# Kernel tuning notes

Measured on AMD Instinct MI355X. Metric: run time of the kernel, lower is better.

Reference implementation:

```python
import jax, jax.numpy as jnp
import numpy as np


def setup_inputs() -> dict:
    key = jax.random.key(0)
    kX, kW, kb, ks = jax.random.split(key, 4)
    B, C, H = 32, 3, 64
    D = C * H * H  # 12288, lin_proj is Linear(D, D)
    N = 196        # superpixels
    X = jax.random.normal(kX, (B, C, H, H), dtype=jnp.float32)
    # scale weight like torch default init (~1/sqrt(D)) to keep activations sane
    W = jax.random.normal(kW, (D, D), dtype=jnp.float32) * (1.0 / np.sqrt(D))
    b = jax.random.normal(kb, (D,), dtype=jnp.float32) * 0.01
    seg_map = jax.random.randint(ks, (B, H, H), 0, N, dtype=jnp.int32)
    return {"X": X, "W": W, "b": b, "seg_map": seg_map, "superpixels": N}


def reference(X, W, b, seg_map, superpixels):
    B, C, H, Wd = X.shape
    D = C * H * Wd
    # lin_proj over the fully flattened image (as in the torch module)
    x = X.reshape(B, D) @ W.T + b                      # [B, D]
    x = x.reshape(B, C, H * Wd)                        # back to per-pixel channels
    pix = x.transpose(0, 2, 1).reshape(B * H * Wd, C)  # [B*HW, C]
    # offset segment ids so every image gets its own id range
    ids = (seg_map.reshape(B, H * Wd) + jnp.arange(B, dtype=seg_map.dtype)[:, None] * superpixels).reshape(-1)
    nseg = B * superpixels
    sums = jax.ops.segment_sum(pix, ids, num_segments=nseg)                     # [B*N, C]
    cnts = jax.ops.segment_sum(jnp.ones((ids.shape[0],), x.dtype), ids, num_segments=nseg)
    means = sums / jnp.maximum(cnts, 1.0)[:, None]     # masked mean per superpixel per channel
    return means.reshape(B, superpixels, C)            # [B, N_superpixels, in_chans]
```

## Files before the change

### kernel.cpp

```cpp
#include <hip/hip_runtime.h>


#include <hip/hip_bf16.h>

typedef __attribute__((ext_vector_type(8))) short short8;
typedef __attribute__((ext_vector_type(4))) float f32x4;

namespace {
constexpr int BATCH = 32;
constexpr int CH    = 3;
constexpr int HWPIX = 4096;
constexpr int DDIM  = 12288;
constexpr int KDIM  = 12288;
constexpr int NSEG  = 196;

constexpr int ROWS = 64;
constexpr int BK   = 128;
}

__device__ __forceinline__ unsigned pkbf16(float lo, float hi) {
    __hip_bfloat162 h = __float22bfloat162_rn(make_float2(lo, hi));
    union { __hip_bfloat162 h2; unsigned u; } c; c.h2 = h; return c.u;
}

__device__ __forceinline__ void gload16(const void* g, void* l) {
    __builtin_amdgcn_global_load_lds(
        (const __attribute__((address_space(1))) void*)g,
        (__attribute__((address_space(3))) void*)l, 16, 0, 0);
}

__global__ __launch_bounds__(256) void convert_x_kernel(
    const float* __restrict__ X, ushort* __restrict__ Xb)
{
    const int i = (blockIdx.x * 256 + threadIdx.x) * 4;
    const float4 v = *reinterpret_cast<const float4*>(X + i);
    union { unsigned u[2]; ushort4 q; } o;
    o.u[0] = pkbf16(v.x, v.y);
    o.u[1] = pkbf16(v.z, v.w);
    *reinterpret_cast<ushort4*>(Xb + i) = o.q;
}

template<int KSPLIT>
__global__ __launch_bounds__(256, 2) void gemm_kernel(
    const float* __restrict__ Wg, const ushort* __restrict__ Xb,
    float* __restrict__ xpart)
{
    constexpr int KRANGE = KDIM / KSPLIT;
    constexpr int NTILE  = KRANGE / BK;

    __shared__ float  wl[2][ROWS * BK];
    __shared__ ushort xl[2][BATCH * BK];

    const int t    = threadIdx.x;
    const int lane = t & 63;
    const int w    = t >> 6;
    const int d0   = blockIdx.x * ROWS;
    const int kb   = blockIdx.y * KRANGE;

    f32x4 acc[2];
#pragma unroll
    for (int nt = 0; nt < 2; ++nt) acc[nt] = (f32x4)(0.f);

#define STAGE(buf, tile)                                                     \
    {                                                                        \
        const int k0 = kb + (tile) * BK;                                     \
        _Pragma("unroll")                                                    \
        for (int i = 0; i < 8; ++i) {                                        \
            const int r  = w * 16 + i * 2 + (lane >> 5);                     \
            const int cs = (lane & 31) ^ (r & 7);                            \
            gload16(Wg + (size_t)(d0 + r) * KDIM + k0 + cs * 4,              \
                    &wl[buf][(w * 16 + i * 2) * BK]);                        \
        }                                                                    \
        _Pragma("unroll")                                                    \
        for (int i = 0; i < 2; ++i) {                                        \
            const int xr = w * 8 + i * 4 + (lane >> 4);                      \
            const int cs = (lane & 15) ^ (xr & 7);                           \
            gload16(Xb + (size_t)xr * KDIM + k0 + cs * 8,                    \
                    &xl[buf][(w * 8 + i * 4) * BK]);                         \
        }                                                                    \
    }

#define COMPUTE(buf)                                                         \
    {                                                                        \
        _Pragma("unroll")                                                    \
        for (int kk = 0; kk < 4; ++kk) {                                     \
            const int R  = w * 16 + (lane & 15);                             \
            const int c0 = kk * 8 + (lane >> 4) * 2;      \
            const float4 f0 = *reinterpret_cast<const float4*>(              \
                &wl[buf][R * BK + (((c0    ) ^ (R & 7)) & 31) * 4]);         \
            const float4 f1 = *reinterpret_cast<const float4*>(              \
                &wl[buf][R * BK + (((c0 + 1) ^ (R & 7)) & 31) * 4]);         \
            union { unsigned u[4]; short8 s8; } A;                           \
            A.u[0] = pkbf16(f0.x, f0.y);                                     \
            A.u[1] = pkbf16(f0.z, f0.w);                                     \
            A.u[2] = pkbf16(f1.x, f1.y);                                     \
            A.u[3] = pkbf16(f1.z, f1.w);                                     \
            _Pragma("unroll")                                                \
            for (int nt = 0; nt < 2; ++nt) {                                 \
                const int b  = nt * 16 + (lane & 15);                        \
                const int xc = (kk * 4 + (lane >> 4)) ^ (b & 7);             \
                const short8 bb = *reinterpret_cast<const short8*>(          \
                    &xl[buf][b * BK + xc * 8]);                              \
                acc[nt] = __builtin_amdgcn_mfma_f32_16x16x32_bf16(           \
                    A.s8, bb, acc[nt], 0, 0, 0);                             \
            }                                                                \
        }                                                                    \
    }

    STAGE(0, 0)
    STAGE(1, 1)
    for (int tile = 0; tile < NTILE; ++tile) {
        const int cur = tile & 1;
        if (tile + 1 < NTILE) {
            asm volatile("s_waitcnt vmcnt(10)" ::: "memory");
        } else {
            asm volatile("s_waitcnt vmcnt(0)" ::: "memory");
        }
        __builtin_amdgcn_s_barrier();
        asm volatile("" ::: "memory");
        COMPUTE(cur)
        asm volatile("s_waitcnt lgkmcnt(0)" ::: "memory");
        __builtin_amdgcn_s_barrier();
        asm volatile("" ::: "memory");
        if (tile + 2 < NTILE) STAGE(cur, tile + 2)
    }
#undef STAGE
#undef COMPUTE

    float* xp = xpart + (size_t)blockIdx.y * BATCH * DDIM;
#pragma unroll
    for (int nt = 0; nt < 2; ++nt) {
        const int b = nt * 16 + (lane & 15);
        const int m = d0 + w * 16 + (lane >> 4) * 4;
#pragma unroll
        for (int r = 0; r < 4; ++r)
            xp[(size_t)b * DDIM + m + r] = acc[nt][r];
    }
}

template<int KSPLIT>
__global__ __launch_bounds__(256) void aggregate_kernel(
    const float* __restrict__ xpart, const float* __restrict__ bias,
    const int* __restrict__ seg, float* __restrict__ out)
{
    __shared__ float sums[NSEG];
    __shared__ int   hist[NSEG];
    const int b = blockIdx.x / CH;
    const int c = blockIdx.x % CH;
    for (int i = threadIdx.x; i < NSEG; i += 256) { sums[i] = 0.f; hist[i] = 0; }
    __syncthreads();
    const size_t base = (size_t)b * DDIM + c * HWPIX;
#pragma unroll
    for (int it = 0; it < HWPIX / 1024; ++it) {
        const int p0 = it * 1024 + threadIdx.x * 4;
        const int4 s4 = *reinterpret_cast<const int4*>(seg + b * HWPIX + p0);
        float4 v = *reinterpret_cast<const float4*>(bias + c * HWPIX + p0);
#pragma unroll
        for (int ks = 0; ks < KSPLIT; ++ks) {
            const float4 xv = *reinterpret_cast<const float4*>(
                xpart + (size_t)ks * BATCH * DDIM + base + p0);
            v.x += xv.x; v.y += xv.y; v.z += xv.z; v.w += xv.w;
        }
        atomicAdd(&hist[s4.x], 1); atomicAdd(&sums[s4.x], v.x);
        atomicAdd(&hist[s4.y], 1); atomicAdd(&sums[s4.y], v.y);
        atomicAdd(&hist[s4.z], 1); atomicAdd(&sums[s4.z], v.z);
        atomicAdd(&hist[s4.w], 1); atomicAdd(&sums[s4.w], v.w);
    }
    __syncthreads();
    for (int s = threadIdx.x; s < NSEG; s += 256)
        out[(b * NSEG + s) * CH + c] = sums[s] / fmaxf((float)hist[s], 1.f);
}

extern "C" void kernel_launch(void* const* d_in, const int* in_sizes, int n_in,
                              void* d_out, int out_size, void* d_ws, size_t ws_size,
                              hipStream_t stream) {
    const float* X    = (const float*)d_in[0];
    const float* W    = (const float*)d_in[1];
    const float* bias = (const float*)d_in[2];
    const int*   seg  = (const int*)d_in[3];
    float* out = (float*)d_out;

    ushort* Xb    = (ushort*)d_ws;
    float*  xpart = (float*)(Xb + (size_t)BATCH * KDIM);

    convert_x_kernel<<<BATCH * KDIM / (256 * 4), 256, 0, stream>>>(X, Xb);

    const size_t base_ws = (size_t)BATCH * KDIM * 2;
    const size_t part_ws = (size_t)BATCH * DDIM * 4;
    if (ws_size >= base_ws + 8 * part_ws) {
        dim3 grid(DDIM / ROWS, 8);
        gemm_kernel<8><<<grid, 256, 0, stream>>>(W, Xb, xpart);
        aggregate_kernel<8><<<BATCH * CH, 256, 0, stream>>>(xpart, bias, seg, out);
    } else {
        dim3 grid(DDIM / ROWS, 4);
        gemm_kernel<4><<<grid, 256, 0, stream>>>(W, Xb, xpart);
        aggregate_kernel<4><<<BATCH * CH, 256, 0, stream>>>(xpart, bias, seg, out);
    }
}
```

Measured before the change: 132.7 us.

## Replace grid-level split-K with in-block per-wave K split and LDS reduction

The GEMM drops the global split-K grid dimension and its partial-sum buffers. Each block now owns 16 output rows, and its four waves each walk an interleaved quarter of K with private double-buffered LDS tiles and no block barriers in the main loop. The waves then reduce their results through shared memory and write a single output, so the aggregate kernel reads one array instead of summing 4-8 partials. This removes partial-sum global traffic and per-tile barriers, but the X tile is re-read per block (768 blocks instead of 192x8) and each wave does less MFMA work per load.

```diff
diff --git a/kernel.cpp b/kernel.cpp
--- a/kernel.cpp
+++ b/kernel.cpp
@@ -14,8 +14,10 @@
 constexpr int KDIM  = 12288;
 constexpr int NSEG  = 196;
 
-constexpr int ROWS = 64;
-constexpr int BK   = 128;
+constexpr int ROWS = 16;
+constexpr int BK   = 64;
+constexpr int NCH  = KDIM / BK;
+constexpr int PERW = NCH / 4;
 }
 
 __device__ __forceinline__ unsigned pkbf16(float lo, float hi) {
@@ -40,56 +42,51 @@
     *reinterpret_cast<ushort4*>(Xb + i) = o.q;
 }
 
-template<int KSPLIT>
 __global__ __launch_bounds__(256, 2) void gemm_kernel(
     const float* __restrict__ Wg, const ushort* __restrict__ Xb,
-    float* __restrict__ xpart)
+    float* __restrict__ x)
 {
-    constexpr int KRANGE = KDIM / KSPLIT;
-    constexpr int NTILE  = KRANGE / BK;
+    __shared__ float  wl[4][2][ROWS * BK];
+    __shared__ ushort xl[4][2][BATCH * BK];
+    __shared__ float  red[4][ROWS][BATCH];
 
-    __shared__ float  wl[2][ROWS * BK];
-    __shared__ ushort xl[2][BATCH * BK];
-
-    const int t    = threadIdx.x;
-    const int lane = t & 63;
-    const int w    = t >> 6;
+    const int lane = threadIdx.x & 63;
+    const int w    = threadIdx.x >> 6;
     const int d0   = blockIdx.x * ROWS;
-    const int kb   = blockIdx.y * KRANGE;
 
     f32x4 acc[2];
 #pragma unroll
     for (int nt = 0; nt < 2; ++nt) acc[nt] = (f32x4)(0.f);
 
-#define STAGE(buf, tile)                                                     \
+#define STAGE(buf, c)                                                        \
     {                                                                        \
-        const int k0 = kb + (tile) * BK;                                     \
+        const int k0 = (c) * BK;                                             \
         _Pragma("unroll")                                                    \
-        for (int i = 0; i < 8; ++i) {                                        \
-            const int r  = w * 16 + i * 2 + (lane >> 5);                     \
-            const int cs = (lane & 31) ^ (r & 7);                            \
+        for (int i = 0; i < 4; ++i) {                                        \
+            const int r  = i * 4 + (lane >> 4);                              \
+            const int cs = (lane & 15) ^ (r & 7);                            \
             gload16(Wg + (size_t)(d0 + r) * KDIM + k0 + cs * 4,              \
-                    &wl[buf][(w * 16 + i * 2) * BK]);                        \
+                    &wl[w][buf][i * 4 * BK]);                                \
         }                                                                    \
         _Pragma("unroll")                                                    \
-        for (int i = 0; i < 2; ++i) {                                        \
-            const int xr = w * 8 + i * 4 + (lane >> 4);                      \
-            const int cs = (lane & 15) ^ (xr & 7);                           \
+        for (int i = 0; i < 4; ++i) {                                        \
+            const int xr = i * 8 + (lane >> 3);                              \
+            const int cs = (lane & 7) ^ (xr & 7);                            \
             gload16(Xb + (size_t)xr * KDIM + k0 + cs * 8,                    \
-                    &xl[buf][(w * 8 + i * 4) * BK]);                         \
+                    &xl[w][buf][i * 8 * BK]);                                \
         }                                                                    \
     }
 
 #define COMPUTE(buf)                                                         \
     {                                                                        \
         _Pragma("unroll")                                                    \
-        for (int kk = 0; kk < 4; ++kk) {                                     \
-            const int R  = w * 16 + (lane & 15);                             \
+        for (int kk = 0; kk < 2; ++kk) {                                     \
+            const int R  = lane & 15;                                        \
             const int c0 = kk * 8 + (lane >> 4) * 2;      \
             const float4 f0 = *reinterpret_cast<const float4*>(              \
-                &wl[buf][R * BK + (((c0    ) ^ (R & 7)) & 31) * 4]);         \
+                &wl[w][buf][R * BK + ((c0    ) ^ (R & 7)) * 4]);             \
             const float4 f1 = *reinterpret_cast<const float4*>(              \
-                &wl[buf][R * BK + (((c0 + 1) ^ (R & 7)) & 31) * 4]);         \
+                &wl[w][buf][R * BK + ((c0 + 1) ^ (R & 7)) * 4]);             \
             union { unsigned u[4]; short8 s8; } A;                           \
             A.u[0] = pkbf16(f0.x, f0.y);                                     \
             A.u[1] = pkbf16(f0.z, f0.w);                                     \
@@ -97,50 +94,56 @@
             A.u[3] = pkbf16(f1.z, f1.w);                                     \
             _Pragma("unroll")                                                \
             for (int nt = 0; nt < 2; ++nt) {                                 \
-                const int b  = nt * 16 + (lane & 15);                        \
-                const int xc = (kk * 4 + (lane >> 4)) ^ (b & 7);             \
+                const int b = nt * 16 + (lane & 15);                         \
+                const int s = kk * 4 + (lane >> 4);                          \
                 const short8 bb = *reinterpret_cast<const short8*>(          \
-                    &xl[buf][b * BK + xc * 8]);                              \
+                    &xl[w][buf][b * BK + (s ^ (b & 7)) * 8]);                \
                 acc[nt] = __builtin_amdgcn_mfma_f32_16x16x32_bf16(           \
                     A.s8, bb, acc[nt], 0, 0, 0);                             \
             }                                                                \
         }                                                                    \
     }
 
-    STAGE(0, 0)
-    STAGE(1, 1)
-    for (int tile = 0; tile < NTILE; ++tile) {
-        const int cur = tile & 1;
-        if (tile + 1 < NTILE) {
-            asm volatile("s_waitcnt vmcnt(10)" ::: "memory");
+    STAGE(0, w)
+    STAGE(1, w + 4)
+    for (int i = 0; i < PERW; ++i) {
+        const int cur = i & 1;
+        if (i + 1 < PERW) {
+            asm volatile("s_waitcnt vmcnt(8)" ::: "memory");
         } else {
             asm volatile("s_waitcnt vmcnt(0)" ::: "memory");
         }
-        __builtin_amdgcn_s_barrier();
-        asm volatile("" ::: "memory");
+        __builtin_amdgcn_sched_barrier(0);
         COMPUTE(cur)
         asm volatile("s_waitcnt lgkmcnt(0)" ::: "memory");
-        __builtin_amdgcn_s_barrier();
-        asm volatile("" ::: "memory");
-        if (tile + 2 < NTILE) STAGE(cur, tile + 2)
+        __builtin_amdgcn_sched_barrier(0);
+        if (i + 2 < PERW) STAGE(cur, w + 4 * (i + 2))
     }
 #undef STAGE
 #undef COMPUTE
 
-    float* xp = xpart + (size_t)blockIdx.y * BATCH * DDIM;
 #pragma unroll
     for (int nt = 0; nt < 2; ++nt) {
-        const int b = nt * 16 + (lane & 15);
-        const int m = d0 + w * 16 + (lane >> 4) * 4;
+        const int b  = nt * 16 + (lane & 15);
+        const int r0 = (lane >> 4) * 4;
 #pragma unroll
         for (int r = 0; r < 4; ++r)
-            xp[(size_t)b * DDIM + m + r] = acc[nt][r];
+            red[w][r0 + r][b] = acc[nt][r];
+    }
+    __syncthreads();
+#pragma unroll
+    for (int h = 0; h < 2; ++h) {
+        const int idx = h * 256 + threadIdx.x;
+        const int b   = idx >> 4;
+        const int r   = idx & 15;
+        const float s = red[0][r][b] + red[1][r][b]
+                      + red[2][r][b] + red[3][r][b];
+        x[(size_t)b * DDIM + d0 + r] = s;
     }
 }
 
-template<int KSPLIT>
 __global__ __launch_bounds__(256) void aggregate_kernel(
-    const float* __restrict__ xpart, const float* __restrict__ bias,
+    const float* __restrict__ x, const float* __restrict__ bias,
     const int* __restrict__ seg, float* __restrict__ out)
 {
     __shared__ float sums[NSEG];
@@ -155,12 +158,8 @@
         const int p0 = it * 1024 + threadIdx.x * 4;
         const int4 s4 = *reinterpret_cast<const int4*>(seg + b * HWPIX + p0);
         float4 v = *reinterpret_cast<const float4*>(bias + c * HWPIX + p0);
-#pragma unroll
-        for (int ks = 0; ks < KSPLIT; ++ks) {
-            const float4 xv = *reinterpret_cast<const float4*>(
-                xpart + (size_t)ks * BATCH * DDIM + base + p0);
-            v.x += xv.x; v.y += xv.y; v.z += xv.z; v.w += xv.w;
-        }
+        const float4 xv = *reinterpret_cast<const float4*>(x + base + p0);
+        v.x += xv.x; v.y += xv.y; v.z += xv.z; v.w += xv.w;
         atomicAdd(&hist[s4.x], 1); atomicAdd(&sums[s4.x], v.x);
         atomicAdd(&hist[s4.y], 1); atomicAdd(&sums[s4.y], v.y);
         atomicAdd(&hist[s4.z], 1); atomicAdd(&sums[s4.z], v.z);
@@ -180,20 +179,10 @@
     const int*   seg  = (const int*)d_in[3];
     float* out = (float*)d_out;
 
-    ushort* Xb    = (ushort*)d_ws;
-    float*  xpart = (float*)(Xb + (size_t)BATCH * KDIM);
+    ushort* Xb = (ushort*)d_ws;
+    float*  x  = (float*)(Xb + (size_t)BATCH * KDIM);
 
     convert_x_kernel<<<BATCH * KDIM / (256 * 4), 256, 0, stream>>>(X, Xb);
-
-    const size_t base_ws = (size_t)BATCH * KDIM * 2;
-    const size_t part_ws = (size_t)BATCH * DDIM * 4;
-    if (ws_size >= base_ws + 8 * part_ws) {
-        dim3 grid(DDIM / ROWS, 8);
-        gemm_kernel<8><<<grid, 256, 0, stream>>>(W, Xb, xpart);
-        aggregate_kernel<8><<<BATCH * CH, 256, 0, stream>>>(xpart, bias, seg, out);
-    } else {
-        dim3 grid(DDIM / ROWS, 4);
-        gemm_kernel<4><<<grid, 256, 0, stream>>>(W, Xb, xpart);
-        aggregate_kernel<4><<<BATCH * CH, 256, 0, stream>>>(xpart, bias, seg, out);
-    }
+    gemm_kernel<<<DDIM / ROWS, 256, 0, stream>>>(W, Xb, x);
+    aggregate_kernel<<<BATCH * CH, 256, 0, stream>>>(x, bias, seg, out);
 }
```

New measurement: 151.1 us. 13.9% more time.
